# Kernel optimization log

Measured on AMD Instinct MI355X. Metric: run time of the kernel, lower is better.

The kernel has to match this reference:

```python
import jax, jax.numpy as jnp
import numpy as np

B, R, S, C, H, MLP = 4, 32, 4, 128, 4, 512  # batch, resolution, box_size, dim, heads, mlp_dim
N = S ** 3            # tokens per window = 64
NW = (R // S) ** 3    # windows per batch element = 512
SHIFT = S // 2


def _layernorm(x, g, b):
    m = jnp.mean(x, axis=-1, keepdims=True)
    v = jnp.var(x, axis=-1, keepdims=True)
    return (x - m) * jax.lax.rsqrt(v + 1e-5) * g + b


def _box_partition(x):
    # x: (b, R, R, R, C) -> (b*NW, N, C)
    b = x.shape[0]
    x = x.reshape(b, R // S, S, R // S, S, R // S, S, C)
    x = x.transpose(0, 1, 3, 5, 2, 4, 6, 7)
    return x.reshape(-1, N, C)


def _box_reverse(w, b):
    # w: (b*NW, N, C) -> (b, R, R, R, C)
    x = w.reshape(b, R // S, R // S, R // S, S, S, S, C)
    x = x.transpose(0, 1, 4, 2, 5, 3, 6, 7)
    return x.reshape(b, R, R, R, C)


def setup_inputs():
    key = jax.random.key(0)
    ks = jax.random.split(key, 8)
    f = lambda k, sh: jax.random.normal(k, sh, dtype=jnp.float32) * 0.02
    x = jax.random.normal(ks[0], (B, R ** 3, C), dtype=jnp.float32)
    qkv_w = f(ks[1], (3 * C, C))
    rpb_table = f(ks[2], ((3 * S - 1) ** 3, H))
    proj_w = f(ks[3], (C, C))
    proj_b = jnp.zeros((C,), jnp.float32)
    norm1_g = jnp.ones((C,), jnp.float32)
    norm1_b = jnp.zeros((C,), jnp.float32)
    norm2_g = jnp.ones((C,), jnp.float32)
    norm2_b = jnp.zeros((C,), jnp.float32)
    mlp_w1 = f(ks[4], (MLP, C))
    mlp_b1 = jnp.zeros((MLP,), jnp.float32)
    mlp_w2 = f(ks[5], (C, MLP))
    mlp_b2 = jnp.zeros((C,), jnp.float32)
    # relative position index (N, N), int constant
    coords = np.stack(np.meshgrid(*([np.arange(S)] * 3), indexing='ij')).reshape(3, -1)
    rel = coords[:, :, None] - coords[:, None, :]
    rel = rel.transpose(1, 2, 0) + (S - 1)
    rel[..., 0] *= (2 * S - 1) ** 2
    rel[..., 1] *= (2 * S - 1)
    rel_index = jnp.asarray(rel.sum(-1), jnp.int32)
    # shifted-window additive attention mask (NW, N, N)
    img = np.zeros((1, R, R, R, 1), np.float32)
    sl = (slice(0, -S), slice(-S, -SHIFT), slice(-SHIFT, None))
    cnt = 0
    for a in sl:
        for b2 in sl:
            for c in sl:
                img[:, a, b2, c, :] = cnt
                cnt += 1
    m = img.reshape(1, R // S, S, R // S, S, R // S, S, 1)
    m = m.transpose(0, 1, 3, 5, 2, 4, 6, 7).reshape(-1, N)
    am = m[:, None, :] - m[:, :, None]
    attn_mask = jnp.asarray(np.where(am != 0, -100.0, 0.0).astype(np.float32))
    return dict(x=x, qkv_w=qkv_w, rpb_table=rpb_table, proj_w=proj_w, proj_b=proj_b,
                norm1_g=norm1_g, norm1_b=norm1_b, norm2_g=norm2_g, norm2_b=norm2_b,
                mlp_w1=mlp_w1, mlp_b1=mlp_b1, mlp_w2=mlp_w2, mlp_b2=mlp_b2,
                attn_mask=attn_mask, rel_index=rel_index)


def reference(x, qkv_w, rpb_table, proj_w, proj_b, norm1_g, norm1_b,
              norm2_g, norm2_b, mlp_w1, mlp_b1, mlp_w2, mlp_b2,
              attn_mask, rel_index):
    scale = (C // H) ** -0.5
    shortcut = x
    xn = _layernorm(x, norm1_g, norm1_b).reshape(B, R, R, R, C)
    xs = jnp.roll(xn, (-SHIFT,) * 3, axis=(1, 2, 3))
    w = _box_partition(xs)  # (B*NW, N, C)
    qkv = (w @ qkv_w.T).reshape(-1, N, 3, H, C // H).transpose(2, 0, 3, 1, 4)
    q, k, v = qkv[0] * scale, qkv[1], qkv[2]  # (B*NW, H, N, hd)
    attn = jnp.einsum('whnd,whmd->whnm', q, k)
    bias = rpb_table[rel_index].transpose(2, 0, 1)  # (H, N, N)
    attn = attn + bias[None]
    attn = attn.reshape(B, NW, H, N, N) + attn_mask[None, :, None]
    attn = jax.nn.softmax(attn.reshape(-1, H, N, N), axis=-1)
    out = jnp.einsum('whnm,whmd->whnd', attn, v).transpose(0, 2, 1, 3).reshape(-1, N, C)
    out = out @ proj_w.T + proj_b
    xm = _box_reverse(out, B)
    xm = jnp.roll(xm, (SHIFT,) * 3, axis=(1, 2, 3)).reshape(B, -1, C)
    x1 = shortcut + 0.5 * xm
    h = _layernorm(x1, norm2_g, norm2_b)
    h = jax.nn.gelu(h @ mlp_w1.T + mlp_b1, approximate=False) @ mlp_w2.T + mlp_b2
    return x1 + 0.5 * h
```

## Files before the change

### kernel.cpp

```cpp
#include <hip/hip_runtime.h>
#include <hip/hip_bf16.h>

typedef unsigned short u16;
typedef unsigned int u32;
typedef short bf16x8 __attribute__((ext_vector_type(8)));
typedef float f32x4 __attribute__((ext_vector_type(4)));

__device__ __forceinline__ u16 f2bf(float f) {
  union { float f; u32 i; } v; v.f = f;
  u32 x = v.i;
  x += 0x7fff + ((x >> 16) & 1);
  return (u16)(x >> 16);
}
__device__ __forceinline__ u32 pack2(float a, float b) {
  return (u32)f2bf(a) | ((u32)f2bf(b) << 16);
}
__device__ __forceinline__ u32 cvtpk2(float a, float b) {
  __hip_bfloat162 t = __float22bfloat162_rn(float2{a, b});
  union { __hip_bfloat162 h; u32 u; } v; v.h = t; return v.u;
}


__global__ void prep_kernel(const float* __restrict__ rpb, const int* __restrict__ rel,
                            const float* __restrict__ qkv_w, const float* __restrict__ proj_w,
                            const float* __restrict__ w1, const float* __restrict__ w2,
                            float* __restrict__ bias, u16* __restrict__ qkv_f,
                            u16* __restrict__ proj_f, u16* __restrict__ w1f,
                            u16* __restrict__ w2f) {
  const int bid = blockIdx.x;
  if (bid < 64) {
    const int idx = bid * 256 + threadIdx.x;
    const int h = idx >> 12, rm = idx & 4095;
    bias[idx] = rpb[rel[rm] * 4 + h];
    return;
  }
  const int i4 = (bid - 64) * 256 + threadIdx.x;
  const int e = i4 * 4;
  const float scale = 0.17677669529663687f;
  float4 v; u16* dst;
  if (e < 49152) {
    v = *(const float4*)(qkv_w + e);
    if (e < 16384) { v.x *= scale; v.y *= scale; v.z *= scale; v.w *= scale; }
    const int row = e >> 7, col = e & 127;
    const int tile = (row >> 4) * 4 + (col >> 5);
    const int lane = ((col >> 3) & 3) * 16 + (row & 15);
    dst = qkv_f + tile * 512 + lane * 8 + (col & 7);
  } else if (e < 65536) {
    const int le = e - 49152;
    v = *(const float4*)(proj_w + le);
    const int row = le >> 7, col = le & 127;
    const int tile = (row >> 4) * 4 + (col >> 5);
    const int lane = ((col >> 3) & 3) * 16 + (row & 15);
    dst = proj_f + tile * 512 + lane * 8 + (col & 7);
  } else if (e < 131072) {
    const int le = e - 65536;
    v = *(const float4*)(w1 + le);
    const int row = le >> 7, col = le & 127;
    const int tile = (row >> 4) * 4 + (col >> 5);
    const int lane = ((col >> 3) & 3) * 16 + (row & 15);
    dst = w1f + tile * 512 + lane * 8 + (col & 7);
  } else {
    const int le = e - 131072;
    v = *(const float4*)(w2 + le);
    const int row = le >> 9, col = le & 511;
    const int tile = (row >> 4) * 16 + (col >> 5);
    const int lane = ((col >> 3) & 3) * 16 + (row & 15);
    dst = w2f + tile * 512 + lane * 8 + (col & 7);
  }
  *(uint2*)dst = make_uint2(pack2(v.x, v.y), pack2(v.z, v.w));
}

__global__ __launch_bounds__(512, 4) void attn_kernel(
    const float* __restrict__ x, const u16* __restrict__ qkv_f,
    const u16* __restrict__ proj_f, const float* __restrict__ proj_b,
    const float* __restrict__ n1g, const float* __restrict__ n1b,
    const float* __restrict__ amask, const float* __restrict__ bias,
    float* __restrict__ out)
{
  __shared__ __align__(16) unsigned char lds[70656];
  __shared__ int srcIdx[64];
  u16* xw = (u16*)(lds);
  u16* qb = (u16*)(lds + 17408);
  u16* kb = (u16*)(lds + 34816);
  u16* vt = (u16*)(lds + 52224);
  unsigned char* Pb = lds;
  u16* Ob = kb;

  const int tid = threadIdx.x;
  const int wv = tid >> 6, lane = tid & 63;
  const int l15 = lane & 15, lg = lane >> 4;
  const int hw = wv & 3;
  const int half = wv >> 2;

  const int wIdx = blockIdx.x;
  const int bb = wIdx >> 9, ww = wIdx & 511;
  const int w0 = ww >> 6, w1i = (ww >> 3) & 7, w2i = ww & 7;

  {
    const int tok = tid >> 3;
    const int qt = tid & 7;
    const int s0 = tok >> 4, s1 = (tok >> 2) & 3, s2 = tok & 3;
    const int p0 = (w0 * 4 + s0 + 2) & 31;
    const int p1 = (w1i * 4 + s1 + 2) & 31;
    const int p2 = (w2i * 4 + s2 + 2) & 31;
    const int src = (bb << 15) + (p0 << 10) + (p1 << 5) + p2;
    if (qt == 0) srcIdx[tok] = src;
    float v[16]; float s = 0.f, sq = 0.f;
    const float4* p4 = (const float4*)(x + src * 128 + qt * 16);
    #pragma unroll
    for (int i = 0; i < 4; ++i) {
      float4 u = p4[i];
      v[i * 4 + 0] = u.x; v[i * 4 + 1] = u.y; v[i * 4 + 2] = u.z; v[i * 4 + 3] = u.w;
      s += u.x + u.y + u.z + u.w;
      sq += u.x * u.x + u.y * u.y + u.z * u.z + u.w * u.w;
    }
    s  += __shfl_xor(s, 1);  s  += __shfl_xor(s, 2);  s  += __shfl_xor(s, 4);
    sq += __shfl_xor(sq, 1); sq += __shfl_xor(sq, 2); sq += __shfl_xor(sq, 4);
    const float mean = s * 0.0078125f;
    const float var  = sq * 0.0078125f - mean * mean;
    const float rstd = rsqrtf(var + 1e-5f);
    u16* dst = xw + tok * 136 + qt * 16;
    #pragma unroll
    for (int i = 0; i < 16; i += 2) {
      const int c = qt * 16 + i;
      float y0 = (v[i]     - mean) * rstd * n1g[c]     + n1b[c];
      float y1 = (v[i + 1] - mean) * rstd * n1g[c + 1] + n1b[c + 1];
      *(u32*)(dst + i) = cvtpk2(y0, y1);
    }
  }
  __syncthreads();

  const f32x4 zero4 = {0.f, 0.f, 0.f, 0.f};

  bf16x8 xa[2][4];
  #pragma unroll
  for (int ti = 0; ti < 2; ++ti)
    #pragma unroll
    for (int ks = 0; ks < 4; ++ks)
      xa[ti][ks] = *(const bf16x8*)(xw + ((half * 2 + ti) * 16 + l15) * 136 + ks * 32 + lg * 8);

  #pragma unroll
  for (int cc = 0; cc < 4; ++cc) {
    const u16* wp = qkv_f + (cc * 4 + hw) * 4 * 512 + lane * 8;
    f32x4 acc[2] = {zero4, zero4};
    #pragma unroll
    for (int ks = 0; ks < 4; ++ks) {
      const bf16x8 bfr = *(const bf16x8*)(wp + ks * 512);
      acc[0] = __builtin_amdgcn_mfma_f32_16x16x32_bf16(bfr, xa[0][ks], acc[0], 0, 0, 0);
      acc[1] = __builtin_amdgcn_mfma_f32_16x16x32_bf16(bfr, xa[1][ks], acc[1], 0, 0, 0);
    }
    u16* dstbuf = (cc < 2) ? qb : kb;
    const int ob = (cc & 1) * 64 + hw * 16 + lg * 4;
    #pragma unroll
    for (int ti = 0; ti < 2; ++ti) {
      const int token = (half * 2 + ti) * 16 + l15;
      uint2 pk = make_uint2(cvtpk2(acc[ti][0], acc[ti][1]), cvtpk2(acc[ti][2], acc[ti][3]));
      *(uint2*)(dstbuf + token * 136 + ob) = pk;
    }
  }
  #pragma unroll
  for (int cc = 4; cc < 6; ++cc) {
    const u16* wp = qkv_f + (cc * 4 + hw) * 4 * 512 + lane * 8;
    f32x4 acc[2] = {zero4, zero4};
    #pragma unroll
    for (int ks = 0; ks < 4; ++ks) {
      const bf16x8 bfr = *(const bf16x8*)(wp + ks * 512);
      acc[0] = __builtin_amdgcn_mfma_f32_16x16x32_bf16(xa[0][ks], bfr, acc[0], 0, 0, 0);
      acc[1] = __builtin_amdgcn_mfma_f32_16x16x32_bf16(xa[1][ks], bfr, acc[1], 0, 0, 0);
    }
    const int cvch = (cc - 4) * 64 + hw * 16 + l15;
    #pragma unroll
    for (int ti = 0; ti < 2; ++ti) {
      uint2 pk = make_uint2(cvtpk2(acc[ti][0], acc[ti][1]), cvtpk2(acc[ti][2], acc[ti][3]));
      *(uint2*)(vt + cvch * 72 + (half * 2 + ti) * 16 + lg * 4) = pk;
    }
  }
  __syncthreads();

  f32x4 s[2][4];
  {
    bf16x8 qa[2];
    #pragma unroll
    for (int ti = 0; ti < 2; ++ti)
      qa[ti] = *(const bf16x8*)(qb + ((half * 2 + ti) * 16 + l15) * 136 + hw * 32 + lg * 8);
    #pragma unroll
    for (int tj = 0; tj < 4; ++tj) {
      const bf16x8 kf = *(const bf16x8*)(kb + (tj * 16 + l15) * 136 + hw * 32 + lg * 8);
      s[0][tj] = __builtin_amdgcn_mfma_f32_16x16x32_bf16(qa[0], kf, zero4, 0, 0, 0);
      s[1][tj] = __builtin_amdgcn_mfma_f32_16x16x32_bf16(qa[1], kf, zero4, 0, 0, 0);
    }
  }
  #pragma unroll
  for (int ti = 0; ti < 2; ++ti) {
    #pragma unroll
    for (int r = 0; r < 4; ++r) {
      const int row = (half * 2 + ti) * 16 + lg * 4 + r;
      const float* bp = bias + hw * 4096 + row * 64;
      const float* mp = amask + ww * 4096 + row * 64;
      #pragma unroll
      for (int tj = 0; tj < 4; ++tj) {
        const int col = tj * 16 + l15;
        s[ti][tj][r] += bp[col] + mp[col];
      }
    }
  }
  __syncthreads();

  unsigned char* ps = Pb + wv * 4096;
  #pragma unroll
  for (int ti = 0; ti < 2; ++ti) {
    #pragma unroll
    for (int r = 0; r < 4; ++r) {
      float mx = fmaxf(fmaxf(s[ti][0][r], s[ti][1][r]), fmaxf(s[ti][2][r], s[ti][3][r]));
      mx = fmaxf(mx, __shfl_xor(mx, 1));
      mx = fmaxf(mx, __shfl_xor(mx, 2));
      mx = fmaxf(mx, __shfl_xor(mx, 4));
      mx = fmaxf(mx, __shfl_xor(mx, 8));
      float sum = 0.f;
      #pragma unroll
      for (int tj = 0; tj < 4; ++tj) {
        float e = __expf(s[ti][tj][r] - mx);
        s[ti][tj][r] = e; sum += e;
      }
      sum += __shfl_xor(sum, 1);
      sum += __shfl_xor(sum, 2);
      sum += __shfl_xor(sum, 4);
      sum += __shfl_xor(sum, 8);
      const float rcp = 1.0f / sum;
      const int row = ti * 16 + lg * 4 + r;
      const int swz = (row & 7) << 4;
      #pragma unroll
      for (int tj = 0; tj < 4; ++tj) {
        const int byteoff = (row * 128 + (tj * 16 + l15) * 2) ^ swz;
        *(u16*)(ps + byteoff) = f2bf(s[ti][tj][r] * rcp);
      }
    }
  }

  {
    f32x4 oacc[2][2] = {{zero4, zero4}, {zero4, zero4}};
    #pragma unroll
    for (int ks = 0; ks < 2; ++ks) {
      bf16x8 pa[2], vb[2];
      #pragma unroll
      for (int ti = 0; ti < 2; ++ti) {
        const int row = ti * 16 + l15;
        const int slot = ((ks * 4 + lg) ^ (row & 7)) << 4;
        pa[ti] = *(const bf16x8*)(ps + row * 128 + slot);
      }
      #pragma unroll
      for (int tj = 0; tj < 2; ++tj)
        vb[tj] = *(const bf16x8*)(vt + (hw * 32 + tj * 16 + l15) * 72 + ks * 32 + lg * 8);
      #pragma unroll
      for (int ti = 0; ti < 2; ++ti)
        #pragma unroll
        for (int tj = 0; tj < 2; ++tj)
          oacc[ti][tj] = __builtin_amdgcn_mfma_f32_16x16x32_bf16(vb[tj], pa[ti], oacc[ti][tj], 0, 0, 0);
    }
    #pragma unroll
    for (int ti = 0; ti < 2; ++ti)
      #pragma unroll
      for (int tj = 0; tj < 2; ++tj) {
        const int token = (half * 2 + ti) * 16 + l15;
        uint2 pk = make_uint2(cvtpk2(oacc[ti][tj][0], oacc[ti][tj][1]),
                              cvtpk2(oacc[ti][tj][2], oacc[ti][tj][3]));
        *(uint2*)(Ob + token * 136 + hw * 32 + tj * 16 + lg * 4) = pk;
      }
  }
  __syncthreads();

  bf16x8 oafr[2][4];
  #pragma unroll
  for (int ti = 0; ti < 2; ++ti)
    #pragma unroll
    for (int ks = 0; ks < 4; ++ks)
      oafr[ti][ks] = *(const bf16x8*)(Ob + ((half * 2 + ti) * 16 + l15) * 136 + ks * 32 + lg * 8);
  #pragma unroll
  for (int cc = 0; cc < 2; ++cc) {
    const u16* wp = proj_f + (cc * 4 + hw) * 4 * 512 + lane * 8;
    f32x4 acc[2] = {zero4, zero4};
    #pragma unroll
    for (int ks = 0; ks < 4; ++ks) {
      const bf16x8 bfr = *(const bf16x8*)(wp + ks * 512);
      acc[0] = __builtin_amdgcn_mfma_f32_16x16x32_bf16(bfr, oafr[0][ks], acc[0], 0, 0, 0);
      acc[1] = __builtin_amdgcn_mfma_f32_16x16x32_bf16(bfr, oafr[1][ks], acc[1], 0, 0, 0);
    }
    const int cb = cc * 64 + hw * 16 + lg * 4;
    const float4 pb4 = *(const float4*)(proj_b + cb);
    #pragma unroll
    for (int ti = 0; ti < 2; ++ti) {
      const int token = (half * 2 + ti) * 16 + l15;
      const int src = srcIdx[token];
      float4 xr = *(const float4*)(x + src * 128 + cb);
      xr.x += 0.5f * (acc[ti][0] + pb4.x);
      xr.y += 0.5f * (acc[ti][1] + pb4.y);
      xr.z += 0.5f * (acc[ti][2] + pb4.z);
      xr.w += 0.5f * (acc[ti][3] + pb4.w);
      *(float4*)(out + src * 128 + cb) = xr;
    }
  }
}

__global__ __launch_bounds__(256, 4) void mlp_kernel(
    const u16* __restrict__ w1f, const float* __restrict__ b1,
    const u16* __restrict__ w2f, const float* __restrict__ b2,
    const float* __restrict__ n2g, const float* __restrict__ n2b,
    float* __restrict__ out)
{
  __shared__ __align__(16) unsigned char lds[35840];
  u16* xn  = (u16*)(lds);
  u16* h1c0 = (u16*)(lds + 17408);
  u16* h1c1 = (u16*)(lds + 26624);

  const int tid = threadIdx.x;
  const int wave = tid >> 6, lane = tid & 63;
  const int l15 = lane & 15, lg = lane >> 4;
  const int base = blockIdx.x * 64;
  const f32x4 zero4 = {0.f, 0.f, 0.f, 0.f};

  {
    const int tl = tid >> 2;
    const int qt = tid & 3;
    const int tokg = base + tl;
    float v[32]; float s = 0.f, sq = 0.f;
    const float4* p4 = (const float4*)(out + tokg * 128 + qt * 32);
    #pragma unroll
    for (int i = 0; i < 8; ++i) {
      float4 u = p4[i];
      v[i * 4 + 0] = u.x; v[i * 4 + 1] = u.y; v[i * 4 + 2] = u.z; v[i * 4 + 3] = u.w;
      s += u.x + u.y + u.z + u.w;
      sq += u.x * u.x + u.y * u.y + u.z * u.z + u.w * u.w;
    }
    s  += __shfl_xor(s, 1);  s  += __shfl_xor(s, 2);
    sq += __shfl_xor(sq, 1); sq += __shfl_xor(sq, 2);
    const float mean = s * 0.0078125f;
    const float var  = sq * 0.0078125f - mean * mean;
    const float rstd = rsqrtf(var + 1e-5f);
    u16* dst = xn + tl * 136 + qt * 32;
    #pragma unroll
    for (int i = 0; i < 32; i += 2) {
      const int c = qt * 32 + i;
      float y0 = (v[i]     - mean) * rstd * n2g[c]     + n2b[c];
      float y1 = (v[i + 1] - mean) * rstd * n2g[c + 1] + n2b[c + 1];
      *(u32*)(dst + i) = cvtpk2(y0, y1);
    }
  }
  __syncthreads();

  f32x4 acc2[4][2];
  #pragma unroll
  for (int ti = 0; ti < 4; ++ti) { acc2[ti][0] = zero4; acc2[ti][1] = zero4; }

  #pragma unroll 1
  for (int oc = 0; oc < 8; ++oc) {
    u16* h1c = (oc & 1) ? h1c1 : h1c0;
    f32x4 a1[4];
    #pragma unroll
    for (int t = 0; t < 4; ++t) a1[t] = zero4;
    const u16* wp1 = w1f + (oc * 4 + wave) * 4 * 512 + lane * 8;
    #pragma unroll
    for (int ks = 0; ks < 4; ++ks) {
      const bf16x8 bfr = *(const bf16x8*)(wp1 + ks * 512);
      #pragma unroll
      for (int ti = 0; ti < 4; ++ti) {
        const bf16x8 afr = *(const bf16x8*)(xn + (ti * 16 + l15) * 136 + ks * 32 + lg * 8);
        a1[ti] = __builtin_amdgcn_mfma_f32_16x16x32_bf16(bfr, afr, a1[ti], 0, 0, 0);
      }
    }
    bf16x8 w2r[2][2];
    #pragma unroll
    for (int tj = 0; tj < 2; ++tj)
      #pragma unroll
      for (int ks = 0; ks < 2; ++ks)
        w2r[tj][ks] = *(const bf16x8*)(w2f + (((wave * 2 + tj) * 16) + (oc * 2 + ks)) * 512 + lane * 8);

    const int olb = wave * 16 + lg * 4;
    const float4 b14 = *(const float4*)(b1 + oc * 64 + olb);
    const float b1v[4] = {b14.x, b14.y, b14.z, b14.w};
    #pragma unroll
    for (int ti = 0; ti < 4; ++ti) {
      float g[4];
      #pragma unroll
      for (int r = 0; r < 4; ++r) {
        const float u = a1[ti][r] + b1v[r];
        const float t = u + 0.044715f * u * u * u;
        g[r] = u / (1.0f + __expf(-1.5957691216057308f * t));
      }
      const int token = ti * 16 + l15;
      *(uint2*)(h1c + token * 72 + olb) = make_uint2(cvtpk2(g[0], g[1]), cvtpk2(g[2], g[3]));
    }
    __syncthreads();

    #pragma unroll
    for (int ks = 0; ks < 2; ++ks) {
      bf16x8 afr[4];
      #pragma unroll
      for (int ti = 0; ti < 4; ++ti)
        afr[ti] = *(const bf16x8*)(h1c + (ti * 16 + l15) * 72 + ks * 32 + lg * 8);
      #pragma unroll
      for (int ti = 0; ti < 4; ++ti)
        #pragma unroll
        for (int tj = 0; tj < 2; ++tj)
          acc2[ti][tj] = __builtin_amdgcn_mfma_f32_16x16x32_bf16(w2r[tj][ks], afr[ti], acc2[ti][tj], 0, 0, 0);
    }
  }

  #pragma unroll
  for (int tj = 0; tj < 2; ++tj) {
    const int cb = wave * 32 + tj * 16 + lg * 4;
    const float4 b24 = *(const float4*)(b2 + cb);
    #pragma unroll
    for (int ti = 0; ti < 4; ++ti) {
      const int tokg = base + ti * 16 + l15;
      float4 o4 = *(float4*)(out + tokg * 128 + cb);
      o4.x += 0.5f * (acc2[ti][tj][0] + b24.x);
      o4.y += 0.5f * (acc2[ti][tj][1] + b24.y);
      o4.z += 0.5f * (acc2[ti][tj][2] + b24.z);
      o4.w += 0.5f * (acc2[ti][tj][3] + b24.w);
      *(float4*)(out + tokg * 128 + cb) = o4;
    }
  }
}

extern "C" void kernel_launch(void* const* d_in, const int* in_sizes, int n_in,
                              void* d_out, int out_size, void* d_ws, size_t ws_size,
                              hipStream_t stream) {
  const float* x      = (const float*)d_in[0];
  const float* qkv_w  = (const float*)d_in[1];
  const float* rpb    = (const float*)d_in[2];
  const float* proj_w = (const float*)d_in[3];
  const float* proj_b = (const float*)d_in[4];
  const float* n1g    = (const float*)d_in[5];
  const float* n1b    = (const float*)d_in[6];
  const float* n2g    = (const float*)d_in[7];
  const float* n2b    = (const float*)d_in[8];
  const float* w1     = (const float*)d_in[9];
  const float* b1     = (const float*)d_in[10];
  const float* w2     = (const float*)d_in[11];
  const float* b2     = (const float*)d_in[12];
  const float* amask  = (const float*)d_in[13];
  const int*   rel    = (const int*)d_in[14];
  float* out  = (float*)d_out;

  unsigned char* ws = (unsigned char*)d_ws;
  float* bias = (float*)(ws);
  u16* qkv_f  = (u16*)(ws + 65536);
  u16* proj_f = (u16*)(ws + 163840);
  u16* w1f    = (u16*)(ws + 196608);
  u16* w2f    = (u16*)(ws + 327680);

  prep_kernel<<<256, 256, 0, stream>>>(rpb, rel, qkv_w, proj_w, w1, w2,
                                       bias, qkv_f, proj_f, w1f, w2f);
  attn_kernel<<<2048, 512, 0, stream>>>(x, qkv_f, proj_f, proj_b, n1g, n1b, amask, bias, out);
  mlp_kernel<<<2048, 256, 0, stream>>>(w1f, b1, w2f, b2, n2g, n2b, out);
}
```

Before: 165.2 us.

## Fuse MLP into attention kernel keeping residual tile in LDS

Merges the MLP stage into the attention kernel so each block computes LayerNorm2, the two MLP GEMMs and the final residual on its own 64-token window. The post-attention residual is kept in shared memory rather than written to and re-read from global memory. This removes a kernel launch and the global round trips of the intermediate activation. In exchange the combined kernel may use more registers and needs extra barriers, and the 8 waves split tokens so weight fragments are loaded twice per block.

```diff
diff --git a/kernel.cpp b/kernel.cpp
--- a/kernel.cpp
+++ b/kernel.cpp
@@ -70,11 +70,14 @@
   *(uint2*)dst = make_uint2(pack2(v.x, v.y), pack2(v.z, v.w));
 }
 
-__global__ __launch_bounds__(512, 4) void attn_kernel(
+__global__ __launch_bounds__(512, 4) void fused_kernel(
     const float* __restrict__ x, const u16* __restrict__ qkv_f,
     const u16* __restrict__ proj_f, const float* __restrict__ proj_b,
     const float* __restrict__ n1g, const float* __restrict__ n1b,
     const float* __restrict__ amask, const float* __restrict__ bias,
+    const u16* __restrict__ w1f, const float* __restrict__ b1,
+    const u16* __restrict__ w2f, const float* __restrict__ b2,
+    const float* __restrict__ n2g, const float* __restrict__ n2b,
     float* __restrict__ out)
 {
   __shared__ __align__(16) unsigned char lds[70656];
@@ -85,6 +88,10 @@
   u16* vt = (u16*)(lds + 52224);
   unsigned char* Pb = lds;
   u16* Ob = kb;
+  float* x1f = (float*)(lds);
+  u16* xn  = (u16*)(lds + 34816);
+  u16* h1c0 = (u16*)(lds + 52224);
+  u16* h1c1 = (u16*)(lds + 61440);
 
   const int tid = threadIdx.x;
   const int wv = tid >> 6, lane = tid & 63;
@@ -296,50 +303,32 @@
       xr.y += 0.5f * (acc[ti][1] + pb4.y);
       xr.z += 0.5f * (acc[ti][2] + pb4.z);
       xr.w += 0.5f * (acc[ti][3] + pb4.w);
-      *(float4*)(out + src * 128 + cb) = xr;
-    }
-  }
-}
-
-__global__ __launch_bounds__(256, 4) void mlp_kernel(
-    const u16* __restrict__ w1f, const float* __restrict__ b1,
-    const u16* __restrict__ w2f, const float* __restrict__ b2,
-    const float* __restrict__ n2g, const float* __restrict__ n2b,
-    float* __restrict__ out)
-{
-  __shared__ __align__(16) unsigned char lds[35840];
-  u16* xn  = (u16*)(lds);
-  u16* h1c0 = (u16*)(lds + 17408);
-  u16* h1c1 = (u16*)(lds + 26624);
-
-  const int tid = threadIdx.x;
-  const int wave = tid >> 6, lane = tid & 63;
-  const int l15 = lane & 15, lg = lane >> 4;
-  const int base = blockIdx.x * 64;
-  const f32x4 zero4 = {0.f, 0.f, 0.f, 0.f};
+      *(float4*)(x1f + token * 132 + cb) = xr;
+    }
+  }
+  __syncthreads();
 
   {
-    const int tl = tid >> 2;
-    const int qt = tid & 3;
-    const int tokg = base + tl;
-    float v[32]; float s = 0.f, sq = 0.f;
-    const float4* p4 = (const float4*)(out + tokg * 128 + qt * 32);
-    #pragma unroll
-    for (int i = 0; i < 8; ++i) {
+    const int tok = tid >> 3;
+    const int qt = tid & 7;
+    float v[16]; float s2 = 0.f, sq = 0.f;
+    const float4* p4 = (const float4*)(x1f + tok * 132 + qt * 16);
+    #pragma unroll
+    for (int i = 0; i < 4; ++i) {
       float4 u = p4[i];
       v[i * 4 + 0] = u.x; v[i * 4 + 1] = u.y; v[i * 4 + 2] = u.z; v[i * 4 + 3] = u.w;
-      s += u.x + u.y + u.z + u.w;
+      s2 += u.x + u.y + u.z + u.w;
       sq += u.x * u.x + u.y * u.y + u.z * u.z + u.w * u.w;
     }
-    s  += __shfl_xor(s, 1);  s  += __shfl_xor(s, 2);
-    sq += __shfl_xor(sq, 1); sq += __shfl_xor(sq, 2);
-    const float mean = s * 0.0078125f;
+    s2 += __shfl_xor(s2, 1); s2 += __shfl_xor(s2, 2); s2 += __shfl_xor(s2, 4);
+    sq += __shfl_xor(sq, 1); sq += __shfl_xor(sq, 2); sq += __shfl_xor(sq, 4);
+    const float mean = s2 * 0.0078125f;
     const float var  = sq * 0.0078125f - mean * mean;
     const float rstd = rsqrtf(var + 1e-5f);
-    u16* dst = xn + tl * 136 + qt * 32;
-    #pragma unroll
-    for (int i = 0; i < 32; i += 2) {
-      const int c = qt * 32 + i;
+    u16* dst = xn + tok * 136 + qt * 16;
+    #pragma unroll
+    for (int i = 0; i < 16; i += 2) {
+      const int c = qt * 16 + i;
       float y0 = (v[i]     - mean) * rstd * n2g[c]     + n2b[c];
       float y1 = (v[i + 1] - mean) * rstd * n2g[c + 1] + n2b[c + 1];
       *(u32*)(dst + i) = cvtpk2(y0, y1);
@@ -347,23 +336,18 @@
   }
   __syncthreads();
 
-  f32x4 acc2[4][2];
-  #pragma unroll
-  for (int ti = 0; ti < 4; ++ti) { acc2[ti][0] = zero4; acc2[ti][1] = zero4; }
-
+  f32x4 acc2[2][2] = {{zero4, zero4}, {zero4, zero4}};
   #pragma unroll 1
   for (int oc = 0; oc < 8; ++oc) {
     u16* h1c = (oc & 1) ? h1c1 : h1c0;
-    f32x4 a1[4];
-    #pragma unroll
-    for (int t = 0; t < 4; ++t) a1[t] = zero4;
-    const u16* wp1 = w1f + (oc * 4 + wave) * 4 * 512 + lane * 8;
+    f32x4 a1[2] = {zero4, zero4};
+    const u16* wp1 = w1f + (oc * 4 + hw) * 4 * 512 + lane * 8;
     #pragma unroll
     for (int ks = 0; ks < 4; ++ks) {
       const bf16x8 bfr = *(const bf16x8*)(wp1 + ks * 512);
       #pragma unroll
-      for (int ti = 0; ti < 4; ++ti) {
-        const bf16x8 afr = *(const bf16x8*)(xn + (ti * 16 + l15) * 136 + ks * 32 + lg * 8);
+      for (int ti = 0; ti < 2; ++ti) {
+        const bf16x8 afr = *(const bf16x8*)(xn + ((half * 2 + ti) * 16 + l15) * 136 + ks * 32 + lg * 8);
         a1[ti] = __builtin_amdgcn_mfma_f32_16x16x32_bf16(bfr, afr, a1[ti], 0, 0, 0);
       }
     }
@@ -372,13 +356,13 @@
     for (int tj = 0; tj < 2; ++tj)
       #pragma unroll
       for (int ks = 0; ks < 2; ++ks)
-        w2r[tj][ks] = *(const bf16x8*)(w2f + (((wave * 2 + tj) * 16) + (oc * 2 + ks)) * 512 + lane * 8);
-
-    const int olb = wave * 16 + lg * 4;
+        w2r[tj][ks] = *(const bf16x8*)(w2f + (((hw * 2 + tj) * 16) + (oc * 2 + ks)) * 512 + lane * 8);
+
+    const int olb = hw * 16 + lg * 4;
     const float4 b14 = *(const float4*)(b1 + oc * 64 + olb);
     const float b1v[4] = {b14.x, b14.y, b14.z, b14.w};
     #pragma unroll
-    for (int ti = 0; ti < 4; ++ti) {
+    for (int ti = 0; ti < 2; ++ti) {
       float g[4];
       #pragma unroll
       for (int r = 0; r < 4; ++r) {
@@ -386,19 +370,19 @@
         const float t = u + 0.044715f * u * u * u;
         g[r] = u / (1.0f + __expf(-1.5957691216057308f * t));
       }
-      const int token = ti * 16 + l15;
+      const int token = (half * 2 + ti) * 16 + l15;
       *(uint2*)(h1c + token * 72 + olb) = make_uint2(cvtpk2(g[0], g[1]), cvtpk2(g[2], g[3]));
     }
     __syncthreads();
 
     #pragma unroll
     for (int ks = 0; ks < 2; ++ks) {
-      bf16x8 afr[4];
-      #pragma unroll
-      for (int ti = 0; ti < 4; ++ti)
-        afr[ti] = *(const bf16x8*)(h1c + (ti * 16 + l15) * 72 + ks * 32 + lg * 8);
-      #pragma unroll
-      for (int ti = 0; ti < 4; ++ti)
+      bf16x8 afr[2];
+      #pragma unroll
+      for (int ti = 0; ti < 2; ++ti)
+        afr[ti] = *(const bf16x8*)(h1c + ((half * 2 + ti) * 16 + l15) * 72 + ks * 32 + lg * 8);
+      #pragma unroll
+      for (int ti = 0; ti < 2; ++ti)
         #pragma unroll
         for (int tj = 0; tj < 2; ++tj)
           acc2[ti][tj] = __builtin_amdgcn_mfma_f32_16x16x32_bf16(w2r[tj][ks], afr[ti], acc2[ti][tj], 0, 0, 0);
@@ -407,17 +391,18 @@
 
   #pragma unroll
   for (int tj = 0; tj < 2; ++tj) {
-    const int cb = wave * 32 + tj * 16 + lg * 4;
+    const int cb = hw * 32 + tj * 16 + lg * 4;
     const float4 b24 = *(const float4*)(b2 + cb);
     #pragma unroll
-    for (int ti = 0; ti < 4; ++ti) {
-      const int tokg = base + ti * 16 + l15;
-      float4 o4 = *(float4*)(out + tokg * 128 + cb);
-      o4.x += 0.5f * (acc2[ti][tj][0] + b24.x);
-      o4.y += 0.5f * (acc2[ti][tj][1] + b24.y);
-      o4.z += 0.5f * (acc2[ti][tj][2] + b24.z);
-      o4.w += 0.5f * (acc2[ti][tj][3] + b24.w);
-      *(float4*)(out + tokg * 128 + cb) = o4;
+    for (int ti = 0; ti < 2; ++ti) {
+      const int token = (half * 2 + ti) * 16 + l15;
+      const int src = srcIdx[token];
+      float4 xr = *(const float4*)(x1f + token * 132 + cb);
+      xr.x += 0.5f * (acc2[ti][tj][0] + b24.x);
+      xr.y += 0.5f * (acc2[ti][tj][1] + b24.y);
+      xr.z += 0.5f * (acc2[ti][tj][2] + b24.z);
+      xr.w += 0.5f * (acc2[ti][tj][3] + b24.w);
+      *(float4*)(out + src * 128 + cb) = xr;
     }
   }
 }
@@ -451,6 +436,6 @@
 
   prep_kernel<<<256, 256, 0, stream>>>(rpb, rel, qkv_w, proj_w, w1, w2,
                                        bias, qkv_f, proj_f, w1f, w2f);
-  attn_kernel<<<2048, 512, 0, stream>>>(x, qkv_f, proj_f, proj_b, n1g, n1b, amask, bias, out);
-  mlp_kernel<<<2048, 256, 0, stream>>>(w1f, b1, w2f, b2, n2g, n2b, out);
-}
+  fused_kernel<<<2048, 512, 0, stream>>>(x, qkv_f, proj_f, proj_b, n1g, n1b, amask, bias,
+                                         w1f, b1, w2f, b2, n2g, n2b, out);
+}
```

Result: faster. 146.1 us (-11.6%).
